# Optimization experiments

Measured on AMD Instinct MI355X. Metric: run time of the kernel, lower is better.

## Reference

```python
import jax, jax.numpy as jnp
import numpy as np
from jax import lax

DT = 1.0 / 120.0
B, T = 4096, 128
TWO_PI = 2.0 * np.pi


def setup_inputs() -> dict:
    key = jax.random.key(0)
    k1, k2, k3, k4 = jax.random.split(key, 4)
    return {
        "params": jax.random.normal(k1, (4,), jnp.float32),
        "covariance_params": jax.random.normal(k2, (7,), jnp.float32),
        "init_states": jax.random.normal(k3, (B, 6), jnp.float32),
        "measurements": jax.random.normal(k4, (B, T, 3), jnp.float32),
    }


def _wrap(a):
    # wrap angle innovation to [-pi, pi]
    return a - TWO_PI * jnp.round(a / TWO_PI)


def _smooth_loss(params, covariance_params, init_state, z):
    # z: [T, 3] measurements of (x, y, theta)
    friction = (jnp.tanh(params[0]) + 1.0) * 0.01
    damping = (jnp.tanh(params[1]) + 1.0) * 0.01
    cp = jax.nn.sigmoid(covariance_params)
    R = jnp.diag(cp[:3])                                    # [3,3] meas noise
    Q = jnp.diag(cp[jnp.array([3, 3, 4, 4, 5, 6])])         # [6,6] proc noise
    I6 = jnp.eye(6, dtype=z.dtype)
    Hm = jnp.zeros((3, 6), z.dtype).at[0, 0].set(1.).at[1, 1].set(1.).at[2, 4].set(1.)
    P0 = 0.01 * I6

    def f_and_F(s):
        # free-sliding puck dynamics: [x, y, dx, dy, th, dth]
        x, y, dx, dy, th, dth = s
        ndx = dx - DT * (damping * dx + friction * jnp.tanh(100. * dx))
        ndy = dy - DT * (damping * dy + friction * jnp.tanh(100. * dy))
        ndth = dth * (1.0 - DT * damping)
        ns = jnp.stack([x + DT * dx, y + DT * dy, ndx, ndy, th + DT * dth, ndth])
        gx = 1.0 - DT * (damping + friction * 100. * (1. - jnp.tanh(100. * dx) ** 2))
        gy = 1.0 - DT * (damping + friction * 100. * (1. - jnp.tanh(100. * dy) ** 2))
        F = (I6.at[0, 2].set(DT).at[1, 3].set(DT).at[4, 5].set(DT)
               .at[2, 2].set(gx).at[3, 3].set(gy).at[5, 5].set(1.0 - DT * damping))
        return ns, F

    def ekf_step(carry, zt):
        s, P = carry
        sp, F = f_and_F(s)
        Pp = F @ P @ F.T + Q
        S = Hm @ Pp @ Hm.T + R
        innov = zt - Hm @ sp
        innov = innov.at[2].set(_wrap(innov[2]))
        K = jnp.linalg.solve(S, Hm @ Pp).T          # Pp H^T S^-1
        s_new = sp + K @ innov
        P_new = (I6 - K @ Hm) @ Pp
        return (s_new, P_new), (s_new, P_new, sp, Pp, F)

    _, (sf, Pf, sp, Pp, Fs) = lax.scan(ekf_step, (init_state, P0), z)

    # RTS backward pass
    def rts_step(carry, inp):
        s_next, P_next = carry
        s_f, P_f, sp_n, Pp_n, F_n = inp
        G = jnp.linalg.solve(Pp_n, F_n @ P_f).T     # P_f F^T Pp^{-1}
        s_s = s_f + G @ (s_next - sp_n)
        P_s = P_f + G @ (P_next - Pp_n) @ G.T
        return (s_s, P_s), (s_s, P_s)

    inp = (sf[:-1], Pf[:-1], sp[1:], Pp[1:], Fs[1:])
    _, (s_sm_head, P_sm_head) = lax.scan(rts_step, (sf[-1], Pf[-1]), inp, reverse=True)
    s_sm = jnp.concatenate([s_sm_head, sf[-1:]], 0)   # [T,6]
    P_sm = jnp.concatenate([P_sm_head, Pf[-1:]], 0)   # [T,6,6]

    # log-lik style loss vs measurements[2:] (as in compute_loss)
    zz, st, Pt = z[2:], s_sm[2:], P_sm[2:]
    Sv = jnp.einsum('ij,tjk,lk->til', Hm, Pt, Hm) + R  # [T-2,3,3] meas-space var
    innov_xy = zz[:, :2] - st[:, :2]
    a = zz[:, 2] - st[:, 4]
    a = jnp.where(a > 1.5 * np.pi, a - TWO_PI, a)
    a = jnp.where(a < -1.5 * np.pi, a + TWO_PI, a)
    innov = jnp.concatenate([innov_xy, a[:, None]], 1)
    sign, logdet = jnp.linalg.slogdet(Sv)
    return jnp.sum(sign * jnp.exp(logdet) + jnp.einsum('ti,tij,tj->t', innov, Sv, innov))


def reference(params, covariance_params, init_states, measurements):
    per_seg = jax.vmap(_smooth_loss, in_axes=(None, None, 0, 0))(
        params, covariance_params, init_states, measurements)
    return jnp.sum(per_seg)
```

## Files before the change

### kernel.cpp

```cpp
#include <hip/hip_runtime.h>
#include <cmath>


namespace {

constexpr int B = 4096;
constexpr int T = 128;
constexpr int NT = B * 3;
constexpr int NBLK1 = 192;
constexpr int TRIPLES = 126 * B;
constexpr float DTc     = 1.0f / 120.0f;
constexpr float TWO_PIc = 6.28318530717958647692f;
constexpr float PI_1_5  = 4.71238898038468985769f;
constexpr float INV_2PI = 0.15915494309189533577f;

__device__ __forceinline__ float frcp(float x) { return __builtin_amdgcn_rcpf(x); }

__device__ __forceinline__ float fast_tanh(float x) {
  float e = __expf(2.0f * x);
  return 1.0f - 2.0f * frcp(e + 1.0f);
}
__device__ __forceinline__ float sigmoidf(float x) {
  return frcp(1.0f + __expf(-x));
}

__global__ __launch_bounds__(64, 1) void chains_kernel(
    const float* __restrict__ params, const float* __restrict__ covp,
    const float* __restrict__ init_states, const float* __restrict__ z,
    float4* __restrict__ hist4, float* __restrict__ hist1,
    float* __restrict__ aqA, float* __restrict__ out) {
  const int lane = threadIdx.x;
  const int blk = blockIdx.x;
  const int f = blk >> 6;
  const int g = blk & 63;
  const int seq = g * 64 + lane;
  const int fi = f * B + seq;

  const float friction = (fast_tanh(params[0]) + 1.0f) * 0.01f;
  const float damping  = (fast_tanh(params[1]) + 1.0f) * 0.01f;
  float cp[7];
#pragma unroll
  for (int i = 0; i < 7; i++) cp[i] = sigmoidf(covp[i]);
  const float dcoef = 1.0f - DTc * damping;
  const bool isTH = (f == 2);
  const float q0 = isTH ? cp[5] : cp[3];
  const float q1 = isTH ? cp[6] : cp[4];
  const float r  = cp[f];

  const int pidx = (f == 0) ? 0 : (f == 1) ? 1 : 4;
  const int vidx = (f == 0) ? 2 : (f == 1) ? 3 : 5;
  float p = init_states[seq * 6 + pidx];
  float v = init_states[seq * 6 + vidx];
  float P00 = 0.01f, P01 = 0.0f, P11 = 0.01f;

  const float* __restrict__ zp = z + (size_t)seq * (T * 3) + f;

  float qacc = 0.0f;

  float zb[8];
#pragma unroll
  for (int i = 0; i < 8; i++) zb[i] = zp[i * 3];

#pragma unroll 8
  for (int t = 0; t < T; t++) {
    const int sl = t & 7;
    const float zc = zb[sl];
    const int tf = (t + 8 < T) ? (t + 8) : (T - 1);
    zb[sl] = zp[tf * 3];

    float gg, tv;
    if (!isTH) {
      const float th = fast_tanh(100.0f * v);
      tv = v - DTc * (damping * v + friction * th);
      gg = 1.0f - DTc * (damping + 100.0f * friction * (1.0f - th * th));
    } else {
      tv = dcoef * v;
      gg = dcoef;
    }
    const float tp = p + DTc * v;
    const float u = P01 + DTc * P11;
    const float Pp00 = P00 + DTc * P01 + DTc * u + q0;
    const float Pp01 = gg * u;
    const float Pp11 = gg * (gg * P11) + q1;
    const float iS = frcp(Pp00 + r);
    const float K0 = Pp00 * iS;
    const float K1 = Pp01 * iS;
    float e = zc - tp;
    if (isTH) e = e - TWO_PIc * rintf(e * INV_2PI);
    p = tp + K0 * e;
    v = tv + K1 * e;
    const float om = 1.0f - K0;
    P00 = om * Pp00;
    P01 = om * Pp01;
    P11 = Pp11 - K1 * Pp01;

    hist4[(size_t)t * NT + fi] = make_float4(p, v, P00, P01);
    hist1[(size_t)t * NT + fi] = P11;
  }

  {
    const float zl = zp[(T - 1) * 3];
    float e = zl - p;
    if (isTH) {
      if (e >  PI_1_5) e -= TWO_PIc;
      if (e < -PI_1_5) e += TWO_PIc;
    }
    const float a = P00 + r;
    qacc += a * e * e;
    aqA[(size_t)((T - 1) * 3 + f) * B + seq] = a;
  }

  float sp_ = p, sv_ = v, Ps00 = P00, Ps01 = P01, Ps11 = P11;

  float4 h4b[8];
  float h1b[8], zbb[8];
#pragma unroll
  for (int i = 0; i < 8; i++) {
    const int n2 = 126 - i;
    h4b[i] = hist4[(size_t)n2 * NT + fi];
    h1b[i] = hist1[(size_t)n2 * NT + fi];
    zbb[i] = zp[n2 * 3];
  }

#pragma unroll 8
  for (int i = 0; i < 128; i++) {
    const int n = 126 - i;
    const int sl = i & 7;
    const float4 h4 = h4b[sl];
    const float h1 = h1b[sl];
    const float zn_ = zbb[sl];
    const int nf = (n >= 10) ? (n - 8) : 2;
    h4b[sl] = hist4[(size_t)nf * NT + fi];
    h1b[sl] = hist1[(size_t)nf * NT + fi];
    zbb[sl] = zp[nf * 3];

    const float fp = h4.x, fv = h4.y, f00 = h4.z, f01 = h4.w, f11 = h1;

    float gg, tv;
    if (!isTH) {
      const float th = fast_tanh(100.0f * fv);
      tv = fv - DTc * (damping * fv + friction * th);
      gg = 1.0f - DTc * (damping + 100.0f * friction * (1.0f - th * th));
    } else {
      tv = dcoef * fv;
      gg = dcoef;
    }
    const float tp = fp + DTc * fv;
    const float u = f01 + DTc * f11;
    const float Pp00 = f00 + DTc * f01 + DTc * u + q0;
    const float Pp01 = gg * u;
    const float Pp11 = gg * (gg * f11) + q1;

    const float idet = frcp(Pp00 * Pp11 - Pp01 * Pp01);
    const float W00 = f00, W01 = DTc * f00 + gg * f01;
    const float W10 = f01, W11 = DTc * f01 + gg * f11;
    const float G00 = (W00 * Pp11 - W01 * Pp01) * idet;
    const float G01 = (W01 * Pp00 - W00 * Pp01) * idet;
    const float G10 = (W10 * Pp11 - W11 * Pp01) * idet;
    const float G11 = (W11 * Pp00 - W10 * Pp01) * idet;

    const float ds0 = sp_ - tp, ds1 = sv_ - tv;
    const float np = fp + G00 * ds0 + G01 * ds1;
    const float nv = fv + G10 * ds0 + G11 * ds1;

    const float M00 = Ps00 - Pp00, M01 = Ps01 - Pp01, M11 = Ps11 - Pp11;
    const float GM00 = G00 * M00 + G01 * M01, GM01 = G00 * M01 + G01 * M11;
    const float GM10 = G10 * M00 + G11 * M01, GM11 = G10 * M01 + G11 * M11;
    Ps00 = f00 + GM00 * G00 + GM01 * G01;
    Ps01 = f01 + GM00 * G10 + GM01 * G11;
    Ps11 = f11 + GM10 * G10 + GM11 * G11;
    sp_ = np;
    sv_ = nv;

    if (n >= 2) {
      const float a = Ps00 + r;
      float e = zn_ - np;
      if (isTH) {
        if (e >  PI_1_5) e -= TWO_PIc;
        if (e < -PI_1_5) e += TWO_PIc;
      }
      qacc += a * e * e;
      aqA[(size_t)(n * 3 + f) * B + seq] = a;
    }
  }

#pragma unroll
  for (int off = 32; off > 0; off >>= 1) qacc += __shfl_down(qacc, off);
  if (lane == 0) atomicAdd(out, qacc);
}

__global__ __launch_bounds__(256, 4) void det_kernel(
    const float* __restrict__ aqA, float* __restrict__ out) {
  const int tid0 = blockIdx.x * 256 + threadIdx.x;
  const int stride = gridDim.x * 256;
  float part = 0.0f;
  for (int idx = tid0; idx < TRIPLES; idx += stride) {
    const int n2 = 2 + (idx >> 12);
    const int seq = idx & (B - 1);
    const float a0 = aqA[(size_t)(n2 * 3 + 0) * B + seq];
    const float a1 = aqA[(size_t)(n2 * 3 + 1) * B + seq];
    const float a2 = aqA[(size_t)(n2 * 3 + 2) * B + seq];
    part += a0 * a1 * a2;
  }
#pragma unroll
  for (int off = 32; off > 0; off >>= 1) part += __shfl_down(part, off);
  __shared__ float red[4];
  if ((threadIdx.x & 63) == 0) red[threadIdx.x >> 6] = part;
  __syncthreads();
  if (threadIdx.x == 0) atomicAdd(out, red[0] + red[1] + red[2] + red[3]);
}

}

extern "C" void kernel_launch(void* const* d_in, const int* in_sizes, int n_in,
                              void* d_out, int out_size, void* d_ws, size_t ws_size,
                              hipStream_t stream) {
  const float* params      = (const float*)d_in[0];
  const float* covp        = (const float*)d_in[1];
  const float* init_states = (const float*)d_in[2];
  const float* z           = (const float*)d_in[3];
  float* out = (float*)d_out;

  const size_t hist4B = (size_t)T * NT * sizeof(float4);
  const size_t hist1B = (size_t)T * NT * sizeof(float);
  const size_t aqB    = (size_t)T * 3 * B * sizeof(float);
  const size_t needBytes = hist4B + hist1B + aqB;

  hipMemsetAsync(d_out, 0, sizeof(float), stream);

  if (ws_size >= needBytes) {
    float4* hist4 = (float4*)d_ws;
    float*  hist1 = (float*)((char*)d_ws + hist4B);
    float*  aqA   = (float*)((char*)d_ws + hist4B + hist1B);
    chains_kernel<<<NBLK1, 64, 0, stream>>>(params, covp, init_states, z,
                                            hist4, hist1, aqA, out);
    det_kernel<<<504, 256, 0, stream>>>(aqA, out);
  }
}
```

Baseline: 123.0 us.

## Parallelize RTS backward pass via affine-operator scan across 16 chunk waves

Splits the fused chain kernel into a forward filter kernel and a backward smoother kernel. The backward RTS recursion is rewritten as composition of affine operators (G, b, C), computed per 8-step chunk by 16 waves and combined with a log-step parallel scan in shared memory, so the serial 127-step dependency becomes mostly parallel. Measurements are also staged through LDS with a padded transpose to coalesce the strided z loads. This adds an extra kernel launch, extra flops for the operator composition, and block-level syncs, and it may change floating-point rounding.

```diff
diff --git a/kernel.cpp b/kernel.cpp
--- a/kernel.cpp
+++ b/kernel.cpp
@@ -7,7 +7,6 @@
 constexpr int B = 4096;
 constexpr int T = 128;
 constexpr int NT = B * 3;
-constexpr int NBLK1 = 192;
 constexpr int TRIPLES = 126 * B;
 constexpr float DTc     = 1.0f / 120.0f;
 constexpr float TWO_PIc = 6.28318530717958647692f;
@@ -24,11 +23,10 @@
   return frcp(1.0f + __expf(-x));
 }
 
-__global__ __launch_bounds__(64, 1) void chains_kernel(
+__global__ __launch_bounds__(64, 1) void fwd_kernel(
     const float* __restrict__ params, const float* __restrict__ covp,
     const float* __restrict__ init_states, const float* __restrict__ z,
-    float4* __restrict__ hist4, float* __restrict__ hist1,
-    float* __restrict__ aqA, float* __restrict__ out) {
+    float4* __restrict__ hist4, float* __restrict__ hist1) {
   const int lane = threadIdx.x;
   const int blk = blockIdx.x;
   const int f = blk >> 6;
@@ -36,6 +34,20 @@
   const int seq = g * 64 + lane;
   const int fi = f * B + seq;
 
+  __shared__ float zl[128 * 65];
+
+  {
+#pragma unroll 4
+    for (int s2 = 0; s2 < 64; s2++) {
+      const float* zb = z + (size_t)(g * 64 + s2) * (T * 3) + f;
+      const float v0 = zb[(size_t)lane * 3];
+      const float v1 = zb[(size_t)(64 + lane) * 3];
+      zl[lane * 65 + s2] = v0;
+      zl[(64 + lane) * 65 + s2] = v1;
+    }
+  }
+  __syncthreads();
+
   const float friction = (fast_tanh(params[0]) + 1.0f) * 0.01f;
   const float damping  = (fast_tanh(params[1]) + 1.0f) * 0.01f;
   float cp[7];
@@ -53,20 +65,9 @@
   float v = init_states[seq * 6 + vidx];
   float P00 = 0.01f, P01 = 0.0f, P11 = 0.01f;
 
-  const float* __restrict__ zp = z + (size_t)seq * (T * 3) + f;
-
-  float qacc = 0.0f;
-
-  float zb[8];
-#pragma unroll
-  for (int i = 0; i < 8; i++) zb[i] = zp[i * 3];
-
 #pragma unroll 8
   for (int t = 0; t < T; t++) {
-    const int sl = t & 7;
-    const float zc = zb[sl];
-    const int tf = (t + 8 < T) ? (t + 8) : (T - 1);
-    zb[sl] = zp[tf * 3];
+    const float zc = zl[t * 65 + lane];
 
     float gg, tv;
     if (!isTH) {
@@ -97,44 +98,60 @@
     hist4[(size_t)t * NT + fi] = make_float4(p, v, P00, P01);
     hist1[(size_t)t * NT + fi] = P11;
   }
+}
+
+__global__ __launch_bounds__(1024, 1) void bwd_kernel(
+    const float* __restrict__ params, const float* __restrict__ covp,
+    const float* __restrict__ z,
+    const float4* __restrict__ hist4, const float* __restrict__ hist1,
+    float* __restrict__ aqA, float* __restrict__ out) {
+  const int tid = threadIdx.x;
+  const int c = tid >> 6;
+  const int j = tid & 63;
+  const int blk = blockIdx.x;
+  const int f = blk >> 6;
+  const int g = blk & 63;
+  const int seq = g * 64 + j;
+  const int fi = f * B + seq;
+
+  __shared__ float ops[16 * 64 * 9];
+  __shared__ float zl[128 * 65];
 
   {
-    const float zl = zp[(T - 1) * 3];
-    float e = zl - p;
-    if (isTH) {
-      if (e >  PI_1_5) e -= TWO_PIc;
-      if (e < -PI_1_5) e += TWO_PIc;
-    }
-    const float a = P00 + r;
-    qacc += a * e * e;
-    aqA[(size_t)((T - 1) * 3 + f) * B + seq] = a;
-  }
-
-  float sp_ = p, sv_ = v, Ps00 = P00, Ps01 = P01, Ps11 = P11;
-
-  float4 h4b[8];
-  float h1b[8], zbb[8];
+#pragma unroll
+    for (int s2 = 0; s2 < 4; s2++) {
+      const int sl_ = c * 4 + s2;
+      const float* zb = z + (size_t)(g * 64 + sl_) * (T * 3) + f;
+      const float v0 = zb[(size_t)j * 3];
+      const float v1 = zb[(size_t)(64 + j) * 3];
+      zl[j * 65 + sl_] = v0;
+      zl[(64 + j) * 65 + sl_] = v1;
+    }
+  }
+
+  const float friction = (fast_tanh(params[0]) + 1.0f) * 0.01f;
+  const float damping  = (fast_tanh(params[1]) + 1.0f) * 0.01f;
+  float cp[7];
+#pragma unroll
+  for (int i = 0; i < 7; i++) cp[i] = sigmoidf(covp[i]);
+  const float dcoef = 1.0f - DTc * damping;
+  const bool isTH = (f == 2);
+  const float q0 = isTH ? cp[5] : cp[3];
+  const float q1 = isTH ? cp[6] : cp[4];
+  const float r  = cp[f];
+
+  float qG00, qG01, qG10, qG11, qb0, qb1, qC00, qC01, qC11;
+  qG00 = qG01 = qG10 = qG11 = qb0 = qb1 = qC00 = qC01 = qC11 = 0.0f;
+  float prG0[8], prG1[8], prB[8], prC[8];
+  bool started = false;
+
 #pragma unroll
   for (int i = 0; i < 8; i++) {
-    const int n2 = 126 - i;
-    h4b[i] = hist4[(size_t)n2 * NT + fi];
-    h1b[i] = hist1[(size_t)n2 * NT + fi];
-    zbb[i] = zp[n2 * 3];
-  }
-
-#pragma unroll 8
-  for (int i = 0; i < 128; i++) {
-    const int n = 126 - i;
-    const int sl = i & 7;
-    const float4 h4 = h4b[sl];
-    const float h1 = h1b[sl];
-    const float zn_ = zbb[sl];
-    const int nf = (n >= 10) ? (n - 8) : 2;
-    h4b[sl] = hist4[(size_t)nf * NT + fi];
-    h1b[sl] = hist1[(size_t)nf * NT + fi];
-    zbb[sl] = zp[nf * 3];
-
-    const float fp = h4.x, fv = h4.y, f00 = h4.z, f01 = h4.w, f11 = h1;
+    const int n = 8 * c + 7 - i;
+    if (n > 126) continue;
+    const float4 h4 = hist4[(size_t)n * NT + fi];
+    const float f11 = hist1[(size_t)n * NT + fi];
+    const float fp = h4.x, fv = h4.y, f00 = h4.z, f01 = h4.w;
 
     float gg, tv;
     if (!isTH) {
@@ -152,41 +169,137 @@
     const float Pp11 = gg * (gg * f11) + q1;
 
     const float idet = frcp(Pp00 * Pp11 - Pp01 * Pp01);
-    const float W00 = f00, W01 = DTc * f00 + gg * f01;
-    const float W10 = f01, W11 = DTc * f01 + gg * f11;
-    const float G00 = (W00 * Pp11 - W01 * Pp01) * idet;
-    const float G01 = (W01 * Pp00 - W00 * Pp01) * idet;
-    const float G10 = (W10 * Pp11 - W11 * Pp01) * idet;
-    const float G11 = (W11 * Pp00 - W10 * Pp01) * idet;
-
-    const float ds0 = sp_ - tp, ds1 = sv_ - tv;
-    const float np = fp + G00 * ds0 + G01 * ds1;
-    const float nv = fv + G10 * ds0 + G11 * ds1;
-
-    const float M00 = Ps00 - Pp00, M01 = Ps01 - Pp01, M11 = Ps11 - Pp11;
-    const float GM00 = G00 * M00 + G01 * M01, GM01 = G00 * M01 + G01 * M11;
-    const float GM10 = G10 * M00 + G11 * M01, GM11 = G10 * M01 + G11 * M11;
-    Ps00 = f00 + GM00 * G00 + GM01 * G01;
-    Ps01 = f01 + GM00 * G10 + GM01 * G11;
-    Ps11 = f11 + GM10 * G10 + GM11 * G11;
-    sp_ = np;
-    sv_ = nv;
-
-    if (n >= 2) {
-      const float a = Ps00 + r;
-      float e = zn_ - np;
-      if (isTH) {
-        if (e >  PI_1_5) e -= TWO_PIc;
-        if (e < -PI_1_5) e += TWO_PIc;
-      }
-      qacc += a * e * e;
-      aqA[(size_t)(n * 3 + f) * B + seq] = a;
-    }
+    const float W01 = DTc * f00 + gg * f01;
+    const float W11 = DTc * f01 + gg * f11;
+    const float G00 = (f00 * Pp11 - W01 * Pp01) * idet;
+    const float G01 = (W01 * Pp00 - f00 * Pp01) * idet;
+    const float G10 = (f01 * Pp11 - W11 * Pp01) * idet;
+    const float G11 = (W11 * Pp00 - f01 * Pp01) * idet;
+    const float b0 = fp - (G00 * tp + G01 * tv);
+    const float b1 = fv - (G10 * tp + G11 * tv);
+    const float Y00 = G00 * Pp00 + G01 * Pp01;
+    const float Y01 = G00 * Pp01 + G01 * Pp11;
+    const float Y10 = G10 * Pp00 + G11 * Pp01;
+    const float Y11 = G10 * Pp01 + G11 * Pp11;
+    const float C00 = f00 - (Y00 * G00 + Y01 * G01);
+    const float C01 = f01 - (Y00 * G10 + Y01 * G11);
+    const float C11 = f11 - (Y10 * G10 + Y11 * G11);
+
+    if (!started) {
+      qG00 = G00; qG01 = G01; qG10 = G10; qG11 = G11;
+      qb0 = b0; qb1 = b1; qC00 = C00; qC01 = C01; qC11 = C11;
+      started = true;
+    } else {
+      const float nG00 = G00 * qG00 + G01 * qG10;
+      const float nG01 = G00 * qG01 + G01 * qG11;
+      const float nG10 = G10 * qG00 + G11 * qG10;
+      const float nG11 = G10 * qG01 + G11 * qG11;
+      const float nb0 = G00 * qb0 + G01 * qb1 + b0;
+      const float nb1 = G10 * qb0 + G11 * qb1 + b1;
+      const float t00 = G00 * qC00 + G01 * qC01;
+      const float t01 = G00 * qC01 + G01 * qC11;
+      const float t10 = G10 * qC00 + G11 * qC01;
+      const float t11 = G10 * qC01 + G11 * qC11;
+      const float nC00 = t00 * G00 + t01 * G01 + C00;
+      const float nC01 = t00 * G10 + t01 * G11 + C01;
+      const float nC11 = t10 * G10 + t11 * G11 + C11;
+      qG00 = nG00; qG01 = nG01; qG10 = nG10; qG11 = nG11;
+      qb0 = nb0; qb1 = nb1; qC00 = nC00; qC01 = nC01; qC11 = nC11;
+    }
+    const int idx = 7 - i;
+    prG0[idx] = qG00; prG1[idx] = qG01; prB[idx] = qb0; prC[idx] = qC00;
+  }
+
+  float* __restrict__ mo = &ops[(c * 64 + j) * 9];
+  mo[0] = qG00; mo[1] = qG01; mo[2] = qG10; mo[3] = qG11;
+  mo[4] = qb0;  mo[5] = qb1;
+  mo[6] = qC00; mo[7] = qC01; mo[8] = qC11;
+  __syncthreads();
+
+#pragma unroll
+  for (int rr = 1; rr < 16; rr <<= 1) {
+    float pv[9];
+    const bool act = (c + rr) < 16;
+    if (act) {
+      const float* __restrict__ pp = &ops[((c + rr) * 64 + j) * 9];
+#pragma unroll
+      for (int k = 0; k < 9; k++) pv[k] = pp[k];
+    }
+    __syncthreads();
+    if (act) {
+      const float nG00 = qG00 * pv[0] + qG01 * pv[2];
+      const float nG01 = qG00 * pv[1] + qG01 * pv[3];
+      const float nG10 = qG10 * pv[0] + qG11 * pv[2];
+      const float nG11 = qG10 * pv[1] + qG11 * pv[3];
+      const float nb0 = qG00 * pv[4] + qG01 * pv[5] + qb0;
+      const float nb1 = qG10 * pv[4] + qG11 * pv[5] + qb1;
+      const float t00 = qG00 * pv[6] + qG01 * pv[7];
+      const float t01 = qG00 * pv[7] + qG01 * pv[8];
+      const float t10 = qG10 * pv[6] + qG11 * pv[7];
+      const float t11 = qG10 * pv[7] + qG11 * pv[8];
+      const float nC00 = t00 * qG00 + t01 * qG01 + qC00;
+      const float nC01 = t00 * qG10 + t01 * qG11 + qC01;
+      const float nC11 = t10 * qG10 + t11 * qG11 + qC11;
+      qG00 = nG00; qG01 = nG01; qG10 = nG10; qG11 = nG11;
+      qb0 = nb0; qb1 = nb1; qC00 = nC00; qC01 = nC01; qC11 = nC11;
+    }
+    mo[0] = qG00; mo[1] = qG01; mo[2] = qG10; mo[3] = qG11;
+    mo[4] = qb0;  mo[5] = qb1;
+    mo[6] = qC00; mo[7] = qC01; mo[8] = qC11;
+    __syncthreads();
+  }
+
+  const float4 ht = hist4[(size_t)(T - 1) * NT + fi];
+  const float ht1 = hist1[(size_t)(T - 1) * NT + fi];
+  float sE0, sE1, PE00, PE01, PE11;
+  float qacc = 0.0f;
+
+  if (c == 15) {
+    sE0 = ht.x; sE1 = ht.y; PE00 = ht.z; PE01 = ht.w; PE11 = ht1;
+    const float a = PE00 + r;
+    float e = zl[(T - 1) * 65 + j] - sE0;
+    if (isTH) {
+      if (e >  PI_1_5) e -= TWO_PIc;
+      if (e < -PI_1_5) e += TWO_PIc;
+    }
+    qacc = a * e * e;
+    aqA[(size_t)((T - 1) * 3 + f) * B + seq] = a;
+  } else {
+    const float* __restrict__ pp = &ops[((c + 1) * 64 + j) * 9];
+    const float eg0 = pp[0], eg1 = pp[1], eg2 = pp[2], eg3 = pp[3];
+    sE0 = eg0 * ht.x + eg1 * ht.y + pp[4];
+    sE1 = eg2 * ht.x + eg3 * ht.y + pp[5];
+    const float Y00 = eg0 * ht.z + eg1 * ht.w;
+    const float Y01 = eg0 * ht.w + eg1 * ht1;
+    const float Y10 = eg2 * ht.z + eg3 * ht.w;
+    const float Y11 = eg2 * ht.w + eg3 * ht1;
+    PE00 = Y00 * eg0 + Y01 * eg1 + pp[6];
+    PE01 = Y00 * eg2 + Y01 * eg3 + pp[7];
+    PE11 = Y10 * eg2 + Y11 * eg3 + pp[8];
+  }
+
+#pragma unroll
+  for (int i = 0; i < 8; i++) {
+    const int n = 8 * c + 7 - i;
+    if (n > 126 || n < 2) continue;
+    const int idx = 7 - i;
+    const float g0 = prG0[idx], g1 = prG1[idx];
+    const float s0n = g0 * sE0 + g1 * sE1 + prB[idx];
+    const float P00n = g0 * g0 * PE00 + 2.0f * g0 * g1 * PE01 +
+                       g1 * g1 * PE11 + prC[idx];
+    const float a = P00n + r;
+    float e = zl[n * 65 + j] - s0n;
+    if (isTH) {
+      if (e >  PI_1_5) e -= TWO_PIc;
+      if (e < -PI_1_5) e += TWO_PIc;
+    }
+    qacc += a * e * e;
+    aqA[(size_t)(n * 3 + f) * B + seq] = a;
   }
 
 #pragma unroll
   for (int off = 32; off > 0; off >>= 1) qacc += __shfl_down(qacc, off);
-  if (lane == 0) atomicAdd(out, qacc);
+  if (j == 0) atomicAdd(out, qacc);
 }
 
 __global__ __launch_bounds__(256, 4) void det_kernel(
@@ -232,8 +345,10 @@
     float4* hist4 = (float4*)d_ws;
     float*  hist1 = (float*)((char*)d_ws + hist4B);
     float*  aqA   = (float*)((char*)d_ws + hist4B + hist1B);
-    chains_kernel<<<NBLK1, 64, 0, stream>>>(params, covp, init_states, z,
-                                            hist4, hist1, aqA, out);
+    fwd_kernel<<<192, 64, 0, stream>>>(params, covp, init_states, z,
+                                       hist4, hist1);
+    bwd_kernel<<<192, 1024, 0, stream>>>(params, covp, z, hist4, hist1,
+                                         aqA, out);
     det_kernel<<<504, 256, 0, stream>>>(aqA, out);
   }
 }
```

After: 154.9 us. +25.9%, slower.
